# Kernel optimization log

Hardware: AMD Instinct MI355X
Metric: run time of the kernel (lower is better)

The kernel has to match this reference:

```python
import jax, jax.numpy as jnp
import numpy as np
from jax import lax

# dims (match init_kwargs / input_specs)
B, CIN, H, W = 32, 32, 48, 160
CL = 32            # out_lstm (per-direction hidden channels)
CO = 64            # out_channels of conv
KH, KW, STRIDE = 2, 2, 2
EPS = 1e-5         # BatchNorm2d eps


def setup_inputs() -> dict:
    key = jax.random.key(0)
    ks = jax.random.split(key, 9)
    s = 0.1
    return {
        "x": jax.random.normal(ks[0], (B, CIN, H, W), jnp.float32),
        # per-direction MDLSTM weights: input proj, left-hidden, top-hidden, bias
        "Wx": jax.random.normal(ks[1], (4, CIN, 5 * CL), jnp.float32) * s,
        "Ul": jax.random.normal(ks[2], (4, CL, 5 * CL), jnp.float32) * s,
        "Ut": jax.random.normal(ks[3], (4, CL, 5 * CL), jnp.float32) * s,
        "bias": jnp.zeros((4, 5 * CL), jnp.float32),
        # conv_0 (the original forward uses conv_0 for all four directions)
        "conv_w": jax.random.normal(ks[4], (CO, CL, KH, KW), jnp.float32) * s,
        "conv_b": jnp.zeros((CO,), jnp.float32),
        # BatchNorm2d affine params (training-mode batch statistics)
        "gamma": jnp.ones((CO,), jnp.float32),
        "beta": jnp.zeros((CO,), jnp.float32),
    }


def _mdlstm_dir(xz, Ul, Ut):
    """One scan direction of a Graves-style 2D MDLSTM.
    xz: [H, W, B, 5C] precomputed input projection (incl. bias).
    Gates order: i, f_left, f_top, o, g. Returns h: [H, W, B, C]."""
    C = Ul.shape[0]
    Bn = xz.shape[2]
    zero_row = jnp.zeros((xz.shape[1], Bn, C), xz.dtype)  # [W, B, C]

    def col_step(carry, inp):
        h_l, c_l = carry                 # [B, C] state from the left
        z_c, h_t, c_t = inp              # per-cell input proj + top state
        z = z_c + h_l @ Ul + h_t @ Ut    # [B, 5C]
        i, fl, ft, o, g = jnp.split(z, 5, axis=-1)
        c = (jax.nn.sigmoid(fl) * c_l + jax.nn.sigmoid(ft) * c_t
             + jax.nn.sigmoid(i) * jnp.tanh(g))
        h = jax.nn.sigmoid(o) * jnp.tanh(c)
        return (h, c), (h, c)

    def row_step(carry, xz_row):
        h_top, c_top = carry             # [W, B, C] previous row states
        init = (jnp.zeros((Bn, C), xz.dtype), jnp.zeros((Bn, C), xz.dtype))
        _, (h_row, c_row) = lax.scan(col_step, init, (xz_row, h_top, c_top))
        return (h_row, c_row), h_row

    _, h_all = lax.scan(row_step, (zero_row, zero_row), xz)  # [H, W, B, C]
    return h_all


def reference(x, Wx, Ul, Ut, bias, conv_w, conv_b, gamma, beta):
    xh = jnp.transpose(x, (2, 3, 0, 1))  # [H, W, B, Cin]
    dirs = []
    for d in range(4):  # 4 scan directions: flip combinations of H / W
        xd = xh
        if d in (1, 3):
            xd = xd[:, ::-1]
        if d in (2, 3):
            xd = xd[::-1]
        # big upfront GEMM: input projection for every cell
        xz = jnp.einsum('hwbc,cd->hwbd', xd, Wx[d]) + bias[d]
        h = _mdlstm_dir(xz, Ul[d], Ut[d])
        if d in (2, 3):
            h = h[::-1]
        if d in (1, 3):
            h = h[:, ::-1]
        dirs.append(h)
    # original applies conv_0 to each direction then sums; conv is linear so
    # conv0(x0)+conv0(x1)+conv0(x2)+conv0(x3) == conv0(x0+x1+x2+x3) + 4*bias
    hsum = dirs[0] + dirs[1] + dirs[2] + dirs[3]           # [H, W, B, C]
    hsum = jnp.transpose(hsum, (2, 3, 0, 1))               # [B, C, H, W]
    y = lax.conv_general_dilated(hsum, conv_w, (STRIDE, STRIDE), 'VALID',
                                 dimension_numbers=('NCHW', 'OIHW', 'NCHW'))
    y = y + (4.0 * conv_b)[None, :, None, None]
    y = jnp.tanh(y)
    # BatchNorm2d, training mode (biased batch variance, eps=1e-5)
    mean = y.mean(axis=(0, 2, 3), keepdims=True)
    var = jnp.square(y - mean).mean(axis=(0, 2, 3), keepdims=True)
    yn = (y - mean) * lax.rsqrt(var + EPS)
    return gamma[None, :, None, None] * yn + beta[None, :, None, None]
```

## Files before the change

### kernel.cpp

```cpp
#include <hip/hip_runtime.h>

typedef __bf16 bf16;
typedef __bf16 bf16x8 __attribute__((ext_vector_type(8)));
typedef float  f32x4  __attribute__((ext_vector_type(4)));
typedef int    i32x2  __attribute__((ext_vector_type(2)));
typedef unsigned long long u64;

#define HH 48
#define WW 160
#define BB 32
#define CINC 32
#define CLC 32
#define COC 64
#define OHH 24
#define OWW 80
#define RD 8
#define SLOT_U64 1280

__device__ __forceinline__ bool probe_bf16(const void* gamma) {
  return ((const unsigned short*)gamma)[0] == 0x3F80;
}
__device__ __forceinline__ float rd_in(const void* p, int idx, bool isb) {
  return isb ? (float)((const bf16*)p)[idx] : ((const float*)p)[idx];
}
__device__ __forceinline__ float fsig(float x) {
  return 1.0f / (1.0f + __expf(-x));
}
__device__ __forceinline__ float ftanh(float x) {
  return 1.0f - 2.0f / (1.0f + __expf(2.0f * x));
}

union PK64 { bf16 h[4]; u64 q; };
union FRU { f32x4 f; bf16x8 v; };

__global__ __launch_bounds__(256) void k_params(const void* __restrict__ bias,
                                                const void* __restrict__ conv_w,
                                                const void* __restrict__ conv_b,
                                                const void* __restrict__ gamma,
                                                const void* __restrict__ beta,
                                                float* __restrict__ biasf,
                                                float* __restrict__ convwT,
                                                float* __restrict__ convbf,
                                                float* __restrict__ gammaf,
                                                float* __restrict__ betaf) {
  bool isb = probe_bf16(gamma);
  int i = blockIdx.x * 256 + threadIdx.x;
  if (i < 640)  biasf[i]  = rd_in(bias, i, isb);
  if (i < 8192) {
    int kk = i >> 11, co = (i >> 5) & 63, cl = i & 31;
    convwT[i] = rd_in(conv_w, co * 128 + cl * 4 + kk, isb);
  }
  if (i < 64) {
    convbf[i] = rd_in(conv_b, i, isb);
    gammaf[i] = rd_in(gamma, i, isb);
    betaf[i]  = rd_in(beta, i, isb);
  }
}

__global__ __launch_bounds__(256) void k_transpose3(const void* __restrict__ x,
                                                    const void* __restrict__ gamma,
                                                    bf16* __restrict__ xT3) {
  bool isb = probe_bf16(gamma);
  int h  = blockIdx.x / 20;
  int w0 = (blockIdx.x % 20) * 8;
  __shared__ float tile[BB * CINC * 8];
  for (int e = threadIdx.x; e < BB * CINC * 8; e += 256) {
    int dw = e & 7, c = (e >> 3) & 31, b = e >> 8;
    tile[e] = rd_in(x, ((b * CINC + c) * HH + h) * WW + w0 + dw, isb);
  }
  __syncthreads();
  const size_t PL = (size_t)HH * WW * 1024;
  for (int e = threadIdx.x; e < BB * CINC * 8; e += 256) {
    int c = e & 31, b = (e >> 5) & 31, dw = e >> 10;
    float v = tile[(b * 32 + c) * 8 + dw];
    bf16 p0 = (bf16)v; float r = v - (float)p0;
    bf16 p1 = (bf16)r;
    bf16 p2 = (bf16)(r - (float)p1);
    size_t base = ((size_t)h * WW + w0 + dw) * 1024 + b * 32 + c;
    xT3[base] = p0; xT3[PL + base] = p1; xT3[2 * PL + base] = p2;
  }
}

#define MF5(Aop, PB, KS)                                                       \
  { _Pragma("unroll") for (int g = 0; g < 5; g++)                              \
      acc[g] = __builtin_amdgcn_mfma_f32_16x16x32_bf16(Aop, Ufr[PB][KS][g],    \
                                                       acc[g], 0, 0, 0); }

__global__ __launch_bounds__(256, 1) void k_mdlstm(
    const bf16* __restrict__ xT3,
    const void* __restrict__ Wx, const void* __restrict__ Ul,
    const void* __restrict__ Ut, const void* __restrict__ gamma_raw,
    const float* __restrict__ biasf,
    u64* __restrict__ ring,
    int* __restrict__ flags,
    int* __restrict__ cons,
    float* __restrict__ planes) {
  bool isb = probe_bf16(gamma_raw);
  int d = blockIdx.x / 48, i = blockIdx.x % 48;
  int fi = d * 48 + i;
  int gh = (d & 2) ? (HH - 1 - i) : i;
  int tid = threadIdx.x;
  int lane = tid & 63, wv = tid >> 6;
  int mtile = wv & 1, hf = wv >> 1, nsub = hf * 16;
  int l15 = lane & 15, quad = lane >> 4;
  int m = mtile * 16 + l15;
  int cl  = nsub + l15;
  int b0q = mtile * 16 + quad * 4;
  int rb = lane & 3;
  int bC = b0q + rb;
  int cl0C = nsub + (l15 & 12);

  __shared__ bf16 Ust[160 * 96];
  __shared__ __align__(16) bf16 Afr[2][3][1024];

  bf16x8 Ufr[3][3][5];
  for (int q = 0; q < 3; q++) {
    for (int e = tid; e < 160 * 96; e += 256) {
      int n = e / 96, k = e % 96;
      float v;
      if (k < 32)      v = rd_in(Ul, (d * 32 + k) * 160 + n, isb);
      else if (k < 64) v = rd_in(Ut, (d * 32 + (k - 32)) * 160 + n, isb);
      else             v = rd_in(Wx, (d * 32 + (k - 64)) * 160 + n, isb);
      bf16 p0 = (bf16)v; float r = v - (float)p0;
      bf16 p1 = (bf16)r;
      Ust[e] = (q == 0) ? p0 : (q == 1) ? p1 : (bf16)(r - (float)p1);
    }
    __syncthreads();
#pragma unroll
    for (int ks = 0; ks < 3; ks++)
#pragma unroll
      for (int g = 0; g < 5; g++)
        Ufr[q][ks][g] =
            *(const bf16x8*)(&Ust[(nsub + 32 * g + l15) * 96 + ks * 32 + quad * 8]);
    __syncthreads();
  }
  float bi[5];
#pragma unroll
  for (int g = 0; g < 5; g++) bi[g] = biasf[d * 160 + 32 * g + nsub + l15];
  for (int e = tid; e < 2 * 3 * 1024; e += 256) (&Afr[0][0][0])[e] = (bf16)0.f;
  __syncthreads();

  float creg[4] = {0.f, 0.f, 0.f, 0.f};

  int fprev = (i > 0)  ? fi - 1 : fi;
  int fnext = (i < 47) ? fi + 1 : fi;
  int* fdst = flags + ((fi << 5) + (mtile << 1) + hf);
  const int* fsrc = flags + ((fprev << 5) + (mtile << 1));
  int* cdst = cons + ((fi << 5) + (mtile << 1) + hf);
  const int* csrc = cons + ((fnext << 5) + (mtile << 1));
  int flag_known = (i > 0) ? -1 : 0x7FFFFFFF;
  int cons_known = -1;
  i32x2 pf;  pf.x = -1;  pf.y = -1;
  i32x2 cpf; cpf.x = -1; cpf.y = -1;

  const int a_rd = m * 64 + ((quad * 16) ^ ((m & 6) << 3));
  const int a_wr = bC * 64 + ((cl0C * 2) ^ ((bC & 6) << 3));

  bf16x8 xreg[3];
  {
    int gw0 = (d & 1) ? (WW - 1) : 0;
#pragma unroll
    for (int p = 0; p < 3; p++)
      xreg[p] = *(const bf16x8*)(xT3 + (size_t)(p * HH + gh) * WW * 1024 +
                                 (size_t)gw0 * 1024 + m * 32 + quad * 8);
  }

  for (int j = 0; j < WW; j++) {
    int gw = (d & 1) ? (WW - 1 - j) : j;

    asm volatile("s_waitcnt vmcnt(0)" : "+v"(pf), "+v"(cpf) :: "memory");
    __builtin_amdgcn_sched_barrier(0);

    if (i < 47) {
      int ck = cpf.x < cpf.y ? cpf.x : cpf.y;
      if (ck > cons_known) cons_known = ck;
      if (j - cons_known > RD) {
        for (;;) {
          i32x2 cv;
          asm volatile("global_load_dwordx2 %0, %1, off sc0 sc1\n\t"
                       "s_waitcnt vmcnt(0)"
                       : "=v"(cv) : "v"(csrc) : "memory");
          int c2 = cv.x < cv.y ? cv.x : cv.y;
          if (c2 > cons_known) cons_known = c2;
          if (j - cons_known <= RD) break;
          __builtin_amdgcn_s_sleep(1);
        }
      }
    }
    if (i > 0 && flag_known < j) {
      int fk = pf.x < pf.y ? pf.x : pf.y;
      if (fk > flag_known) flag_known = fk;
      while (flag_known < j) {
        i32x2 fv2;
        asm volatile("global_load_dwordx2 %0, %1, off sc0 sc1\n\t"
                     "s_waitcnt vmcnt(0)"
                     : "=v"(fv2) : "v"(fsrc) : "memory");
        int f2 = fv2.x < fv2.y ? fv2.x : fv2.y;
        if (f2 > flag_known) flag_known = f2;
        if (flag_known < j) __builtin_amdgcn_s_sleep(1);
      }
    }

    FRU ht0, ht1, ht2, ctq;
    if (i > 0) {
      const char* sb =
          (const char*)(ring + (size_t)((fi - 1) * RD + (j & (RD - 1))) * SLOT_U64);
      const void* a0 = sb + 0 * 2048 + m * 64 + quad * 16;
      const void* a1 = sb + 1 * 2048 + m * 64 + quad * 16;
      const void* a2 = sb + 2 * 2048 + m * 64 + quad * 16;
      const void* a3 = sb + 6144 + (size_t)(cl * 32 + b0q) * 4;
      asm volatile(
          "global_load_dwordx4 %0, %4, off sc0 sc1\n\t"
          "global_load_dwordx4 %1, %5, off sc0 sc1\n\t"
          "global_load_dwordx4 %2, %6, off sc0 sc1\n\t"
          "global_load_dwordx4 %3, %7, off sc0 sc1"
          : "=&v"(ht0.f), "=&v"(ht1.f), "=&v"(ht2.f), "=&v"(ctq.f)
          : "v"(a0), "v"(a1), "v"(a2), "v"(a3)
          : "memory");
    } else {
      ht0.f = ht1.f = ht2.f = ctq.f = (f32x4){0.f, 0.f, 0.f, 0.f};
    }

    const int rbuf = (j + 1) & 1;
    bf16x8 Al[3];
#pragma unroll
    for (int p = 0; p < 3; p++)
      Al[p] = *(const bf16x8*)((const char*)&Afr[rbuf][p][0] + a_rd);

    f32x4 acc[5];
#pragma unroll
    for (int g = 0; g < 5; g++) acc[g] = (f32x4){0.f, 0.f, 0.f, 0.f};
    MF5(Al[0], 0, 0) MF5(Al[0], 1, 0) MF5(Al[1], 0, 0)
    MF5(Al[1], 1, 0) MF5(Al[0], 2, 0) MF5(Al[2], 0, 0)
    MF5(xreg[0], 0, 2) MF5(xreg[0], 1, 2) MF5(xreg[1], 0, 2)
    MF5(xreg[1], 1, 2) MF5(xreg[0], 2, 2) MF5(xreg[2], 0, 2)

    if (i > 0)
      asm volatile("s_waitcnt vmcnt(0)"
                   : "+v"(ht0.f), "+v"(ht1.f), "+v"(ht2.f), "+v"(ctq.f)
                   :: "memory");

    MF5(ht0.v, 0, 1) MF5(ht0.v, 1, 1) MF5(ht1.v, 0, 1)
    MF5(ht1.v, 1, 1) MF5(ht0.v, 2, 1) MF5(ht2.v, 0, 1)

    PK64 myp[3];
#pragma unroll
    for (int r = 0; r < 4; r++) {
      float zi  = acc[0][r] + bi[0];
      float zfl = acc[1][r] + bi[1];
      float zft = acc[2][r] + bi[2];
      float zo  = acc[3][r] + bi[3];
      float zg  = acc[4][r] + bi[4];
      float cv  = fsig(zfl) * creg[r] + fsig(zft) * ctq.f[r] + fsig(zi) * ftanh(zg);
      float hv  = fsig(zo) * ftanh(cv);
      creg[r] = cv;
      bf16 q0 = (bf16)hv; float r1 = hv - (float)q0;
      bf16 q1 = (bf16)r1;
      bf16 q2 = (bf16)(r1 - (float)q1);
      myp[0].h[r] = q0; myp[1].h[r] = q1; myp[2].h[r] = q2;
    }

    int srcb = lane & ~3;
    PK64 outp[3];
#pragma unroll
    for (int p = 0; p < 3; p++) {
      PK64 o;
#pragma unroll
      for (int c = 0; c < 4; c++) {
        PK64 t2; t2.q = __shfl(myp[p].q, srcb + c, 64);
        o.h[c] = t2.h[rb];
      }
      outp[p] = o;
    }

    if (i < 47) {
      u64* slotw = ring + (size_t)(fi * RD + (j & (RD - 1))) * SLOT_U64;
#pragma unroll
      for (int p = 0; p < 3; p++) {
        u64* ha = &slotw[p * 256 + bC * 8 + (cl0C >> 2)];
        asm volatile("global_store_dwordx2 %0, %1, off sc0 sc1"
                     :: "v"(ha), "v"(outp[p].q) : "memory");
      }
      f32x4 cst;
      cst[0] = creg[0]; cst[1] = creg[1]; cst[2] = creg[2]; cst[3] = creg[3];
      u64* ca = &slotw[768 + ((cl * 32 + b0q) >> 1)];
      asm volatile("global_store_dwordx4 %0, %1, off sc0 sc1"
                   :: "v"(ca), "v"(cst) : "memory");
      asm volatile("s_waitcnt vmcnt(0)" ::: "memory");
      if (lane == 0) {
        int fv = j;
        asm volatile("global_store_dword %0, %1, off sc0 sc1"
                     :: "v"(fdst), "v"(fv) : "memory");
      }
    }
    if (i > 0 && (j & 3) == 3 && lane == 0)
      asm volatile("global_store_dword %0, %1, off sc0 sc1"
                   :: "v"(cdst), "v"(j) : "memory");

    {
      f32x4 hp;
#pragma unroll
      for (int c = 0; c < 4; c++)
        hp[c] = (float)outp[0].h[c] + (float)outp[1].h[c] + (float)outp[2].h[c];
      *(f32x4*)(planes + (size_t)((d * HH + gh) * WW + gw) * 1024 + bC * 32 + cl0C) = hp;
    }
    if (j + 1 < WW) {
      int gwn = (d & 1) ? (WW - 2 - j) : (j + 1);
#pragma unroll
      for (int p = 0; p < 3; p++)
        xreg[p] = *(const bf16x8*)(xT3 + (size_t)(p * HH + gh) * WW * 1024 +
                                   (size_t)gwn * 1024 + m * 32 + quad * 8);
    }
    if (i > 0)
      asm volatile("global_load_dwordx2 %0, %1, off sc0 sc1"
                   : "=v"(pf) : "v"(fsrc) : "memory");
    if (i < 47)
      asm volatile("global_load_dwordx2 %0, %1, off sc0 sc1"
                   : "=v"(cpf) : "v"(csrc) : "memory");

#pragma unroll
    for (int p = 0; p < 3; p++)
      *(u64*)((char*)&Afr[j & 1][p][0] + a_wr) = outp[p].q;

    asm volatile("s_waitcnt lgkmcnt(0)" ::: "memory");
    __builtin_amdgcn_s_barrier();
    __builtin_amdgcn_sched_barrier(0);
    asm volatile("" ::: "memory");
  }

  asm volatile("s_waitcnt vmcnt(0)" ::: "memory");
}

__global__ __launch_bounds__(256) void k_conv(const float* __restrict__ planes,
                                              const float* __restrict__ convwT,
                                              const float* __restrict__ convbf,
                                              float* __restrict__ y,
                                              float* __restrict__ sums) {
  int b  = blockIdx.x / OHH;
  int oh = blockIdx.x % OHH;
  __shared__ float hs[2 * WW * 36];
  int tid = threadIdx.x;
  int co = tid >> 2, q = tid & 3;

  f32x4 w4[2][2][8];
#pragma unroll
  for (int kh = 0; kh < 2; kh++)
#pragma unroll
    for (int kw = 0; kw < 2; kw++)
#pragma unroll
      for (int c4 = 0; c4 < 8; c4++)
        w4[kh][kw][c4] =
            *(const f32x4*)(&convwT[(((kh * 2 + kw) * 64 + co) * 32) + 4 * c4]);

  for (int e = tid; e < 2 * WW * CLC; e += 256) {
    int kh = e / (WW * CLC);
    int rem = e % (WW * CLC);
    int w = rem >> 5, cl = rem & 31;
    int h = 2 * oh + kh;
    float v = 0.f;
#pragma unroll
    for (int dd = 0; dd < 4; dd++)
      v += planes[(size_t)((dd * HH + h) * WW + w) * 1024 + b * 32 + cl];
    hs[(kh * WW + w) * 36 + cl] = v;
  }
  __syncthreads();

  float bco = 4.f * convbf[co];
  float s = 0.f, s2 = 0.f;
  for (int mm = 0; mm < 20; mm++) {
    int ow = q + 4 * mm;
    float acc = bco;
#pragma unroll
    for (int kh = 0; kh < 2; kh++)
#pragma unroll
      for (int kw = 0; kw < 2; kw++) {
        const float* hp = &hs[(kh * WW + 2 * ow + kw) * 36];
#pragma unroll
        for (int c4 = 0; c4 < 8; c4++) {
          f32x4 h4 = *(const f32x4*)(hp + 4 * c4);
          acc = fmaf(h4[0], w4[kh][kw][c4][0], acc);
          acc = fmaf(h4[1], w4[kh][kw][c4][1], acc);
          acc = fmaf(h4[2], w4[kh][kw][c4][2], acc);
          acc = fmaf(h4[3], w4[kh][kw][c4][3], acc);
        }
      }
    float v = tanhf(acc);
    y[((b * COC + co) * OHH + oh) * OWW + ow] = v;
    s += v; s2 += v * v;
  }
  s  += __shfl_xor(s, 1);  s  += __shfl_xor(s, 2);
  s2 += __shfl_xor(s2, 1); s2 += __shfl_xor(s2, 2);
  if (q == 0) {
    atomicAdd(&sums[co], s);
    atomicAdd(&sums[64 + co], s2);
  }
}

__global__ __launch_bounds__(256) void k_norm(const float* __restrict__ y,
                                              const float* __restrict__ sums,
                                              const float* __restrict__ gammaf,
                                              const float* __restrict__ betaf,
                                              const void* __restrict__ gamma_raw,
                                              void* __restrict__ out) {
  bool isb = probe_bf16(gamma_raw);
  int e = blockIdx.x * 256 + threadIdx.x;
  int co = (e / (OHH * OWW)) & 63;
  const float inv = 1.0f / (32.0f * OHH * OWW);
  float mean = sums[co] * inv;
  float var  = sums[64 + co] * inv - mean * mean;
  float v = (y[e] - mean) * rsqrtf(var + 1e-5f);
  float r = gammaf[co] * v + betaf[co];
  if (isb) ((bf16*)out)[e] = (bf16)r;
  else     ((float*)out)[e] = r;
}

extern "C" void kernel_launch(void* const* d_in, const int* in_sizes, int n_in,
                              void* d_out, int out_size, void* d_ws, size_t ws_size,
                              hipStream_t stream) {
  const void* x      = d_in[0];
  const void* Wx     = d_in[1];
  const void* Ul     = d_in[2];
  const void* Ut     = d_in[3];
  const void* bias   = d_in[4];
  const void* conv_w = d_in[5];
  const void* conv_b = d_in[6];
  const void* gamma  = d_in[7];
  const void* beta   = d_in[8];

  char* ws = (char*)d_ws;
  bf16*  xT3    = (bf16*)(ws);
  u64*   ring   = (u64*)(ws + 47185920);
  float* y      = (float*)(ws + 47185920);
  float* planes = (float*)(ws + 62914560);
  float* sums   = (float*)(ws + 188743680);
  float* biasf  = (float*)(ws + 188744192);
  float* convwT = (float*)(ws + 188746752);
  float* convbf = (float*)(ws + 188779520);
  float* gammaf = (float*)(ws + 188779776);
  float* betaf  = (float*)(ws + 188780032);
  int*   flags  = (int*)  (ws + 188780288);
  int*   cons   = (int*)  (ws + 188804864);

  hipMemsetAsync(sums, 0, 512, stream);
  hipMemsetAsync(flags, 0xFF, 49152, stream);

  k_params<<<32, 256, 0, stream>>>(bias, conv_w, conv_b, gamma, beta,
                                   biasf, convwT, convbf, gammaf, betaf);
  k_transpose3<<<960, 256, 0, stream>>>(x, gamma, xT3);

  k_mdlstm<<<192, 256, 0, stream>>>(xT3, Wx, Ul, Ut, gamma, biasf,
                                    ring, flags, cons, planes);

  k_conv<<<BB * OHH, 256, 0, stream>>>(planes, convwT, convbf, y, sums);
  k_norm<<<3932160 / 256, 256, 0, stream>>>(y, sums, gammaf, betaf, gamma, d_out);
}
```

Measured before the change: 867.2 us.

## Batch prefetch loads with top-state loads into a single wait per step

Issues the flag, consumer-counter and next-column input prefetch loads alongside the top-neighbour state loads, so a single vmcnt wait covers them all instead of a wait at the top of each step plus another before the top-hidden MFMAs. The LDS write of the new hidden fragment now happens before the flag store's vmcnt wait, and the planes output store becomes an inline-asm non-temporal store placed after the flag store. This shortens the serial per-column critical path of the wavefront-pipelined MDLSTM recurrence. The cost is that the prefetch latency is now exposed on the same wait as the ring loads, and the cross-block flag/counter reads are issued earlier.

Result: slower. 964.1 us (+11.2%).

```diff
diff --git a/kernel.cpp b/kernel.cpp
--- a/kernel.cpp
+++ b/kernel.cpp
@@ -156,20 +156,26 @@
   const int a_rd = m * 64 + ((quad * 16) ^ ((m & 6) << 3));
   const int a_wr = bC * 64 + ((cl0C * 2) ^ ((bC & 6) << 3));
 
-  bf16x8 xreg[3];
+  const size_t PL = (size_t)HH * WW * 1024;
+  const bf16* xrow = xT3 + (size_t)gh * WW * 1024 + m * 32 + quad * 8;
+
+  FRU xc0, xc1, xc2, xn0, xn1, xn2;
   {
     int gw0 = (d & 1) ? (WW - 1) : 0;
-#pragma unroll
-    for (int p = 0; p < 3; p++)
-      xreg[p] = *(const bf16x8*)(xT3 + (size_t)(p * HH + gh) * WW * 1024 +
-                                 (size_t)gw0 * 1024 + m * 32 + quad * 8);
-  }
+    const bf16* xp = xrow + (size_t)gw0 * 1024;
+    asm volatile(
+        "global_load_dwordx4 %0, %3, off\n\t"
+        "global_load_dwordx4 %1, %4, off\n\t"
+        "global_load_dwordx4 %2, %5, off\n\t"
+        "s_waitcnt vmcnt(0)"
+        : "=&v"(xc0.f), "=&v"(xc1.f), "=&v"(xc2.f)
+        : "v"(xp), "v"(xp + PL), "v"(xp + 2 * PL)
+        : "memory");
+  }
+  xn0 = xc0; xn1 = xc1; xn2 = xc2;
 
   for (int j = 0; j < WW; j++) {
     int gw = (d & 1) ? (WW - 1 - j) : j;
-
-    asm volatile("s_waitcnt vmcnt(0)" : "+v"(pf), "+v"(cpf) :: "memory");
-    __builtin_amdgcn_sched_barrier(0);
 
     if (i < 47) {
       int ck = cpf.x < cpf.y ? cpf.x : cpf.y;
@@ -217,8 +223,24 @@
           : "=&v"(ht0.f), "=&v"(ht1.f), "=&v"(ht2.f), "=&v"(ctq.f)
           : "v"(a0), "v"(a1), "v"(a2), "v"(a3)
           : "memory");
+      asm volatile("global_load_dwordx2 %0, %1, off sc0 sc1"
+                   : "=v"(pf) : "v"(fsrc) : "memory");
     } else {
       ht0.f = ht1.f = ht2.f = ctq.f = (f32x4){0.f, 0.f, 0.f, 0.f};
+    }
+    if (i < 47)
+      asm volatile("global_load_dwordx2 %0, %1, off sc0 sc1"
+                   : "=v"(cpf) : "v"(csrc) : "memory");
+    if (j + 1 < WW) {
+      int gwn = (d & 1) ? (WW - 2 - j) : (j + 1);
+      const bf16* xp = xrow + (size_t)gwn * 1024;
+      asm volatile(
+          "global_load_dwordx4 %0, %3, off\n\t"
+          "global_load_dwordx4 %1, %4, off\n\t"
+          "global_load_dwordx4 %2, %5, off"
+          : "=&v"(xn0.f), "=&v"(xn1.f), "=&v"(xn2.f)
+          : "v"(xp), "v"(xp + PL), "v"(xp + 2 * PL)
+          : "memory");
     }
 
     const int rbuf = (j + 1) & 1;
@@ -232,16 +254,18 @@
     for (int g = 0; g < 5; g++) acc[g] = (f32x4){0.f, 0.f, 0.f, 0.f};
     MF5(Al[0], 0, 0) MF5(Al[0], 1, 0) MF5(Al[1], 0, 0)
     MF5(Al[1], 1, 0) MF5(Al[0], 2, 0) MF5(Al[2], 0, 0)
-    MF5(xreg[0], 0, 2) MF5(xreg[0], 1, 2) MF5(xreg[1], 0, 2)
-    MF5(xreg[1], 1, 2) MF5(xreg[0], 2, 2) MF5(xreg[2], 0, 2)
-
-    if (i > 0)
-      asm volatile("s_waitcnt vmcnt(0)"
-                   : "+v"(ht0.f), "+v"(ht1.f), "+v"(ht2.f), "+v"(ctq.f)
-                   :: "memory");
+    MF5(xc0.v, 0, 2) MF5(xc0.v, 1, 2) MF5(xc1.v, 0, 2)
+    MF5(xc1.v, 1, 2) MF5(xc0.v, 2, 2) MF5(xc2.v, 0, 2)
+
+    asm volatile("s_waitcnt vmcnt(0)"
+                 : "+v"(ht0.f), "+v"(ht1.f), "+v"(ht2.f), "+v"(ctq.f),
+                   "+v"(pf), "+v"(cpf), "+v"(xn0.f), "+v"(xn1.f), "+v"(xn2.f)
+                 :: "memory");
 
     MF5(ht0.v, 0, 1) MF5(ht0.v, 1, 1) MF5(ht1.v, 0, 1)
     MF5(ht1.v, 1, 1) MF5(ht0.v, 2, 1) MF5(ht2.v, 0, 1)
+
+    if (j + 1 < WW) { xc0 = xn0; xc1 = xn1; xc2 = xn2; }
 
     PK64 myp[3];
 #pragma unroll
@@ -286,6 +310,12 @@
       u64* ca = &slotw[768 + ((cl * 32 + b0q) >> 1)];
       asm volatile("global_store_dwordx4 %0, %1, off sc0 sc1"
                    :: "v"(ca), "v"(cst) : "memory");
+    }
+#pragma unroll
+    for (int p = 0; p < 3; p++)
+      *(u64*)((char*)&Afr[j & 1][p][0] + a_wr) = outp[p].q;
+
+    if (i < 47) {
       asm volatile("s_waitcnt vmcnt(0)" ::: "memory");
       if (lane == 0) {
         int fv = j;
@@ -302,25 +332,10 @@
 #pragma unroll
       for (int c = 0; c < 4; c++)
         hp[c] = (float)outp[0].h[c] + (float)outp[1].h[c] + (float)outp[2].h[c];
-      *(f32x4*)(planes + (size_t)((d * HH + gh) * WW + gw) * 1024 + bC * 32 + cl0C) = hp;
-    }
-    if (j + 1 < WW) {
-      int gwn = (d & 1) ? (WW - 2 - j) : (j + 1);
-#pragma unroll
-      for (int p = 0; p < 3; p++)
-        xreg[p] = *(const bf16x8*)(xT3 + (size_t)(p * HH + gh) * WW * 1024 +
-                                   (size_t)gwn * 1024 + m * 32 + quad * 8);
-    }
-    if (i > 0)
-      asm volatile("global_load_dwordx2 %0, %1, off sc0 sc1"
-                   : "=v"(pf) : "v"(fsrc) : "memory");
-    if (i < 47)
-      asm volatile("global_load_dwordx2 %0, %1, off sc0 sc1"
-                   : "=v"(cpf) : "v"(csrc) : "memory");
-
-#pragma unroll
-    for (int p = 0; p < 3; p++)
-      *(u64*)((char*)&Afr[j & 1][p][0] + a_wr) = outp[p].q;
+      float* pp = planes + (size_t)((d * HH + gh) * WW + gw) * 1024 + bC * 32 + cl0C;
+      asm volatile("global_store_dwordx4 %0, %1, off nt"
+                   :: "v"(pp), "v"(hp) : "memory");
+    }
 
     asm volatile("s_waitcnt lgkmcnt(0)" ::: "memory");
     __builtin_amdgcn_s_barrier();
```
